# Kernel optimization log

Measured on AMD Instinct MI355X. Metric: run time of the kernel, lower is better.

Reference implementation:

```python
import jax, jax.numpy as jnp
import numpy as np
from jax.ops import segment_sum, segment_max

# Graph layout: B contiguous graphs of NPER nodes each
N, B, NPER, E, K = 32768, 32, 1024, 524288, 32
IN_DIM, HID = 64, 64
H1, H2 = 4, 2
NEG_ATTN, NEG_ACT = 0.2, 0.01  # DGL GATConv leaky slope; module's LeakyReLU slope


def _gat(x, src, dst, W, al, ar, H, D):
    # DGL GATConv, no bias, no residual, dropout=0
    f = (x @ W).reshape(N, H, D)                      # [N,H,D]
    el = jnp.einsum('nhd,hd->nh', f, al)              # src attention term
    er = jnp.einsum('nhd,hd->nh', f, ar)              # dst attention term
    e = jax.nn.leaky_relu(el[src] + er[dst], NEG_ATTN)  # [E,H]
    m = segment_max(e, dst, num_segments=N)
    m = jnp.where(jnp.isfinite(m), m, 0.0)            # guard isolated nodes
    p = jnp.exp(e - m[dst])
    z = segment_sum(p, dst, num_segments=N)
    a = p / jnp.maximum(z[dst], 1e-9)                 # edge softmax over in-edges
    return segment_sum(a[:, :, None] * f[src], dst, num_segments=N)  # [N,H,D]


def _graphnorm(x, alpha, gamma, beta, eps=1e-5):
    # GraphNorm (Cai et al.): per-graph node normalization with learnable mean scale
    xb = x.reshape(B, NPER, *x.shape[1:])
    mean = xb.mean(axis=1, keepdims=True)
    c = xb - alpha * mean
    var = (c * c).mean(axis=1, keepdims=True)
    return (gamma * c / jnp.sqrt(var + eps) + beta).reshape(x.shape)


def _sortpool(x):
    # DGL SortPooling: sort each node's features ascending, pick top-K nodes by last channel
    xs = jnp.sort(x, axis=-1).reshape(B, NPER, -1)
    _, idx = jax.lax.top_k(xs[:, :, -1], K)           # [B,K]
    sel = jnp.take_along_axis(xs, idx[:, :, None], axis=1)  # [B,K,D]
    return sel.reshape(B, -1)


def setup_inputs() -> dict:
    key = jax.random.key(0)
    ks = jax.random.split(key, 16)
    rng = np.random.default_rng(0)
    # edges constrained within each contiguous graph block
    g = rng.integers(0, B, size=E)
    src = (g * NPER + rng.integers(0, NPER, size=E)).astype(np.int32)
    dst = (g * NPER + rng.integers(0, NPER, size=E)).astype(np.int32)
    s = 0.05
    return {
        'features': jax.random.normal(ks[0], (N, IN_DIM), jnp.float32),
        'src': jnp.asarray(src), 'dst': jnp.asarray(dst),
        'W1': jax.random.normal(ks[1], (IN_DIM, H1 * HID), jnp.float32) * s,
        'al1': jax.random.normal(ks[2], (H1, HID), jnp.float32) * s,
        'ar1': jax.random.normal(ks[3], (H1, HID), jnp.float32) * s,
        'W2': jax.random.normal(ks[4], (H1 * HID, H2 * HID), jnp.float32) * s,
        'al2': jax.random.normal(ks[5], (H2, HID), jnp.float32) * s,
        'ar2': jax.random.normal(ks[6], (H2, HID), jnp.float32) * s,
        'gn1_alpha': jnp.ones((HID,), jnp.float32),
        'gn1_gamma': jnp.ones((HID,), jnp.float32),
        'gn1_beta': jnp.zeros((HID,), jnp.float32),
        'gn2_alpha': jnp.ones((HID,), jnp.float32),
        'gn2_gamma': jnp.ones((HID,), jnp.float32),
        'gn2_beta': jnp.zeros((HID,), jnp.float32),
        'fc1_w': jax.random.normal(ks[7], (2 * K * HID, K * HID), jnp.float32) * 0.02,
        'fc1_b': jnp.zeros((K * HID,), jnp.float32),
        'fc2_w': jax.random.normal(ks[8], (K * HID, 16), jnp.float32) * 0.02,
        'fc2_b': jnp.zeros((16,), jnp.float32),
    }


def reference(features, src, dst, W1, al1, ar1, W2, al2, ar2,
              gn1_alpha, gn1_gamma, gn1_beta, gn2_alpha, gn2_gamma, gn2_beta,
              fc1_w, fc1_b, fc2_w, fc2_b):
    h1 = _gat(features, src, dst, W1, al1, ar1, H1, HID)          # [N,4,HID]
    h1 = jax.nn.leaky_relu(_graphnorm(h1, gn1_alpha, gn1_gamma, gn1_beta), NEG_ACT)
    r1 = _sortpool(h1.mean(1))                                    # [B,K*HID]
    h2 = _gat(h1.reshape(N, -1), src, dst, W2, al2, ar2, H2, HID)  # [N,2,HID]
    h2 = jax.nn.leaky_relu(_graphnorm(h2, gn2_alpha, gn2_gamma, gn2_beta), NEG_ACT)
    r = jnp.concatenate([r1, _sortpool(h2.mean(1))], axis=1)      # [B,2*K*HID]
    hidden = jax.nn.relu(r @ fc1_w + fc1_b)
    return hidden @ fc2_w + fc2_b                                 # [B,16]
```

## Files before the change

kernel.cpp:

```cpp
#include <hip/hip_runtime.h>
#include <math.h>

#define NNODES 32768
#define NGRAPH 32
#define NPERG  1024
#define KSEL   32
#define FC1_KS 64

__device__ inline float wave_reduce_sum(float v) {
  #pragma unroll
  for (int off = 32; off > 0; off >>= 1) v += __shfl_xor(v, off, 64);
  return v;
}
__device__ inline float wave_reduce_max(float v) {
  #pragma unroll
  for (int off = 32; off > 0; off >>= 1) v = fmaxf(v, __shfl_xor(v, off, 64));
  return v;
}

__global__ void csr_count(const int* __restrict__ dst, int* __restrict__ counts, int E_) {
  int e = blockIdx.x * 256 + threadIdx.x;
  if (e < E_) atomicAdd(&counts[dst[e]], 1);
}

__global__ __launch_bounds__(1024) void csr_scan(const int* __restrict__ counts,
                                                 int* __restrict__ rowptr,
                                                 int* __restrict__ cursor) {
  __shared__ int partial[1024];
  const int tid = threadIdx.x;
  const int base = tid * 32;
  int c[32];
  int s = 0;
  #pragma unroll
  for (int i = 0; i < 32; ++i) { c[i] = counts[base + i]; s += c[i]; }
  partial[tid] = s;
  __syncthreads();
  for (int off = 1; off < 1024; off <<= 1) {
    int t = (tid >= off) ? partial[tid - off] : 0;
    __syncthreads();
    partial[tid] += t;
    __syncthreads();
  }
  int run = partial[tid] - s;
  #pragma unroll
  for (int i = 0; i < 32; ++i) {
    rowptr[base + i] = run;
    cursor[base + i] = run;
    run += c[i];
  }
  if (tid == 1023) rowptr[NNODES] = run;
}

__global__ void csr_fill(const int* __restrict__ src, const int* __restrict__ dst,
                         int* __restrict__ cursor, int* __restrict__ csrsrc, int E_) {
  int e = blockIdx.x * 256 + threadIdx.x;
  if (e < E_) {
    int p = atomicAdd(&cursor[dst[e]], 1);
    csrsrc[p] = src[e];
  }
}

template <int K, int C, int H>
__global__ __launch_bounds__(256) void gemm_fused(
    const float* __restrict__ X, const float* __restrict__ W,
    const float* __restrict__ al, const float* __restrict__ ar,
    float* __restrict__ F, float* __restrict__ el, float* __restrict__ er) {
  __shared__ float Xs[16][68];
  __shared__ float Ws[16][64];
  __shared__ float redl[64][16];
  __shared__ float redr[64][16];
  const int tid = threadIdx.x;
  const int tx = tid & 15, ty = tid >> 4;
  const int bx = blockIdx.x;
  const int xcd = bx & 7, pos = bx >> 3;
  const int gph = xcd + (pos >> 4) * 8;
  const int row0 = (gph * 16 + (pos & 15)) * 64;
  const int col0 = blockIdx.y * 64;

  float acc[4][4];
  #pragma unroll
  for (int i = 0; i < 4; ++i)
    #pragma unroll
    for (int j = 0; j < 4; ++j) acc[i][j] = 0.f;

  const int rld = tid >> 2;
  const int kq = (tid & 3) * 4;
  const int kw = tid >> 4;
  const int cw = (tid & 15) * 4;

  for (int kt = 0; kt < K; kt += 16) {
    float4 xv = *(const float4*)&X[(size_t)(row0 + rld) * K + kt + kq];
    Xs[kq + 0][rld] = xv.x; Xs[kq + 1][rld] = xv.y;
    Xs[kq + 2][rld] = xv.z; Xs[kq + 3][rld] = xv.w;
    *(float4*)&Ws[kw][cw] = *(const float4*)&W[(size_t)(kt + kw) * C + col0 + cw];
    __syncthreads();
    #pragma unroll
    for (int k = 0; k < 16; ++k) {
      float xr[4], wr[4];
      #pragma unroll
      for (int i = 0; i < 4; ++i) xr[i] = Xs[k][ty * 4 + i];
      #pragma unroll
      for (int j = 0; j < 4; ++j) wr[j] = Ws[k][tx * 4 + j];
      #pragma unroll
      for (int i = 0; i < 4; ++i)
        #pragma unroll
        for (int j = 0; j < 4; ++j) acc[i][j] = fmaf(xr[i], wr[j], acc[i][j]);
    }
    __syncthreads();
  }

  float av[4], rv[4];
  #pragma unroll
  for (int j = 0; j < 4; ++j) { av[j] = al[col0 + tx * 4 + j]; rv[j] = ar[col0 + tx * 4 + j]; }
  #pragma unroll
  for (int i = 0; i < 4; ++i) {
    float4 o = make_float4(acc[i][0], acc[i][1], acc[i][2], acc[i][3]);
    *(float4*)&F[(size_t)(row0 + ty * 4 + i) * C + col0 + tx * 4] = o;
    float pl = acc[i][0] * av[0] + acc[i][1] * av[1] + acc[i][2] * av[2] + acc[i][3] * av[3];
    float pr = acc[i][0] * rv[0] + acc[i][1] * rv[1] + acc[i][2] * rv[2] + acc[i][3] * rv[3];
    redl[ty * 4 + i][tx] = pl;
    redr[ty * 4 + i][tx] = pr;
  }
  __syncthreads();
  if (tid < 64) {
    float s = 0.f, t = 0.f;
    #pragma unroll
    for (int x = 0; x < 16; ++x) { s += redl[tid][x]; t += redr[tid][x]; }
    el[(row0 + tid) * H + blockIdx.y] = s;
    er[(row0 + tid) * H + blockIdx.y] = t;
  }
}

template <int H>
__device__ inline void load_ev(const float* __restrict__ el, int s, float* ev) {
  if constexpr (H == 4) {
    float4 t = *(const float4*)(el + (size_t)s * 4);
    ev[0] = t.x; ev[1] = t.y; ev[2] = t.z; ev[3] = t.w;
  } else {
    float2 t = *(const float2*)(el + (size_t)s * 2);
    ev[0] = t.x; ev[1] = t.y;
  }
}

template <int H>
__global__ __launch_bounds__(256) void gat_agg(
    const float* __restrict__ F, const float* __restrict__ el,
    const float* __restrict__ er, const int* __restrict__ rowptr,
    const int* __restrict__ csrsrc, float* __restrict__ out) {
  __shared__ float plds[4][64][H];
  __shared__ int slds[4][64];
  const int wave = threadIdx.x >> 6;
  const int lane = threadIdx.x & 63;
  const int wg = blockIdx.x;
  const int xcd = wg & 7, pos = wg >> 3;
  const int g = xcd + (pos >> 8) * 8;
  const int n = g * NPERG + (pos & 255) * 4 + wave;
  const int beg = rowptr[n], end = rowptr[n + 1];
  const int hsel = (H == 4) ? (lane >> 4) : (lane >> 5);

  float erh[H];
  #pragma unroll
  for (int h = 0; h < H; ++h) erh[h] = er[n * H + h];

  float accv[H], psum[H];
  #pragma unroll
  for (int h = 0; h < H; ++h) { accv[h] = 0.f; psum[h] = 0.f; }

  for (int cbeg = beg; cbeg < end; cbeg += 64) {
    int cnt = end - cbeg;
    if (cnt > 64) cnt = 64;
    float pv[H];
    int s = 0;
    #pragma unroll
    for (int h = 0; h < H; ++h) pv[h] = 0.f;
    if (lane < cnt) {
      s = csrsrc[cbeg + lane];
      float ev[H];
      load_ev<H>(el, s, ev);
      #pragma unroll
      for (int h = 0; h < H; ++h) {
        float e = ev[h] + erh[h];
        e = e >= 0.f ? e : 0.2f * e;
        pv[h] = __expf(e);
      }
    }
    #pragma unroll
    for (int h = 0; h < H; ++h) psum[h] += wave_reduce_sum(pv[h]);
    slds[wave][lane] = s;
    if constexpr (H == 4)
      *(float4*)&plds[wave][lane][0] = make_float4(pv[0], pv[1], pv[2], pv[3]);
    else
      *(float2*)&plds[wave][lane][0] = make_float2(pv[0], pv[1]);
    __builtin_amdgcn_s_waitcnt(0);

    int j = 0;
    for (; j + 4 <= cnt; j += 4) {
      int ss0 = slds[wave][j + 0], ss1 = slds[wave][j + 1];
      int ss2 = slds[wave][j + 2], ss3 = slds[wave][j + 3];
      float pb0 = plds[wave][j + 0][hsel], pb1 = plds[wave][j + 1][hsel];
      float pb2 = plds[wave][j + 2][hsel], pb3 = plds[wave][j + 3][hsel];
      if constexpr (H == 4) {
        float4 f0 = *(const float4*)&F[(size_t)ss0 * 256 + lane * 4];
        float4 f1 = *(const float4*)&F[(size_t)ss1 * 256 + lane * 4];
        float4 f2 = *(const float4*)&F[(size_t)ss2 * 256 + lane * 4];
        float4 f3 = *(const float4*)&F[(size_t)ss3 * 256 + lane * 4];
        accv[0] = fmaf(pb0, f0.x, accv[0]); accv[1] = fmaf(pb0, f0.y, accv[1]);
        accv[2] = fmaf(pb0, f0.z, accv[2]); accv[3] = fmaf(pb0, f0.w, accv[3]);
        accv[0] = fmaf(pb1, f1.x, accv[0]); accv[1] = fmaf(pb1, f1.y, accv[1]);
        accv[2] = fmaf(pb1, f1.z, accv[2]); accv[3] = fmaf(pb1, f1.w, accv[3]);
        accv[0] = fmaf(pb2, f2.x, accv[0]); accv[1] = fmaf(pb2, f2.y, accv[1]);
        accv[2] = fmaf(pb2, f2.z, accv[2]); accv[3] = fmaf(pb2, f2.w, accv[3]);
        accv[0] = fmaf(pb3, f3.x, accv[0]); accv[1] = fmaf(pb3, f3.y, accv[1]);
        accv[2] = fmaf(pb3, f3.z, accv[2]); accv[3] = fmaf(pb3, f3.w, accv[3]);
      } else {
        float2 f0 = *(const float2*)&F[(size_t)ss0 * 128 + lane * 2];
        float2 f1 = *(const float2*)&F[(size_t)ss1 * 128 + lane * 2];
        float2 f2 = *(const float2*)&F[(size_t)ss2 * 128 + lane * 2];
        float2 f3 = *(const float2*)&F[(size_t)ss3 * 128 + lane * 2];
        accv[0] = fmaf(pb0, f0.x, accv[0]); accv[1] = fmaf(pb0, f0.y, accv[1]);
        accv[0] = fmaf(pb1, f1.x, accv[0]); accv[1] = fmaf(pb1, f1.y, accv[1]);
        accv[0] = fmaf(pb2, f2.x, accv[0]); accv[1] = fmaf(pb2, f2.y, accv[1]);
        accv[0] = fmaf(pb3, f3.x, accv[0]); accv[1] = fmaf(pb3, f3.y, accv[1]);
      }
    }
    for (; j < cnt; ++j) {
      int ss = slds[wave][j];
      float pb = plds[wave][j][hsel];
      if constexpr (H == 4) {
        float4 fv = *(const float4*)&F[(size_t)ss * 256 + lane * 4];
        accv[0] = fmaf(pb, fv.x, accv[0]); accv[1] = fmaf(pb, fv.y, accv[1]);
        accv[2] = fmaf(pb, fv.z, accv[2]); accv[3] = fmaf(pb, fv.w, accv[3]);
      } else {
        float2 fv = *(const float2*)&F[(size_t)ss * 128 + lane * 2];
        accv[0] = fmaf(pb, fv.x, accv[0]); accv[1] = fmaf(pb, fv.y, accv[1]);
      }
    }
  }

  float z;
  if constexpr (H == 4)
    z = hsel == 0 ? psum[0] : hsel == 1 ? psum[1] : hsel == 2 ? psum[2] : psum[3];
  else
    z = hsel == 0 ? psum[0] : psum[1];
  float inv = 1.0f / fmaxf(z, 1e-9f);
  if constexpr (H == 4) {
    float4 o = make_float4(accv[0] * inv, accv[1] * inv, accv[2] * inv, accv[3] * inv);
    *(float4*)&out[(size_t)n * 256 + lane * 4] = o;
  } else {
    float2 o = make_float2(accv[0] * inv, accv[1] * inv);
    *(float2*)&out[(size_t)n * 128 + lane * 2] = o;
  }
}

template <int C>
__global__ void gn_stats_partial(const float* __restrict__ X, float* __restrict__ ps,
                                 float* __restrict__ ps2) {
  const int id = blockIdx.x;
  const int xcd = id & 7, pos = id >> 3;
  const int b = xcd + (pos >> 4) * 8;
  const int sgm = pos & 15;
  int ch = threadIdx.x;
  const float* p = X + ((size_t)b * NPERG + sgm * 64) * C + ch;
  float sx = 0.f, sx2 = 0.f;
  for (int i = 0; i < 64; ++i) { float x = p[(size_t)i * C]; sx += x; sx2 += x * x; }
  ps[(b * 16 + sgm) * C + ch] = sx;
  ps2[(b * 16 + sgm) * C + ch] = sx2;
}

template <int C>
__global__ void gn_stats_final(const float* __restrict__ ps, const float* __restrict__ ps2,
                               const float* __restrict__ alpha, const float* __restrict__ gamma,
                               const float* __restrict__ beta, float* __restrict__ scale,
                               float* __restrict__ shift) {
  int b = blockIdx.x, ch = threadIdx.x;
  float sx = 0.f, sx2 = 0.f;
  for (int s = 0; s < 16; ++s) { sx += ps[(b * 16 + s) * C + ch]; sx2 += ps2[(b * 16 + s) * C + ch]; }
  const float inv = 1.0f / (float)NPERG;
  float mu = sx * inv;
  int d = ch & 63;
  float a = alpha[d];
  float var = sx2 * inv - mu * mu * a * (2.f - a);
  float sc = gamma[d] / sqrtf(var + 1e-5f);
  scale[b * C + ch] = sc;
  shift[b * C + ch] = beta[d] - sc * a * mu;
}

__global__ void gn_apply1(const float* __restrict__ h1, const float* __restrict__ scale,
                          const float* __restrict__ shift, float* __restrict__ h1n,
                          float* __restrict__ keyb) {
  const int wg = blockIdx.x;
  const int xcd = wg & 7, pos = wg >> 3;
  const int g = xcd + (pos >> 8) * 8;
  const int n = g * NPERG + (pos & 255) * 4 + (threadIdx.x >> 6);
  const int d = threadIdx.x & 63;
  const int b = g;
  float s = 0.f;
  #pragma unroll
  for (int h = 0; h < 4; ++h) {
    int ch = h * 64 + d;
    float y = scale[b * 256 + ch] * h1[(size_t)n * 256 + ch] + shift[b * 256 + ch];
    y = y >= 0.f ? y : 0.01f * y;
    h1n[(size_t)n * 256 + ch] = y;
    s += y;
  }
  float key = wave_reduce_max(0.25f * s);
  if (d == 0) keyb[n] = key;
}

__global__ void gn_apply2(const float* __restrict__ h2, const float* __restrict__ scale,
                          const float* __restrict__ shift, float* __restrict__ keyb) {
  const int wg = blockIdx.x;
  const int xcd = wg & 7, pos = wg >> 3;
  const int g = xcd + (pos >> 8) * 8;
  const int n = g * NPERG + (pos & 255) * 4 + (threadIdx.x >> 6);
  const int d = threadIdx.x & 63;
  const int b = g;
  float s = 0.f;
  #pragma unroll
  for (int h = 0; h < 2; ++h) {
    int ch = h * 64 + d;
    float y = scale[b * 128 + ch] * h2[(size_t)n * 128 + ch] + shift[b * 128 + ch];
    y = y >= 0.f ? y : 0.01f * y;
    s += y;
  }
  float key = wave_reduce_max(0.5f * s);
  if (d == 0) keyb[n] = key;
}

__device__ inline float bitonic_sort64(float v, int lane) {
  #pragma unroll
  for (int kk = 2; kk <= 64; kk <<= 1) {
    #pragma unroll
    for (int j = kk >> 1; j > 0; j >>= 1) {
      float o = __shfl_xor(v, j, 64);
      bool lower = (lane & j) == 0;
      bool asc = (lane & kk) == 0;
      v = (lower == asc) ? fminf(v, o) : fmaxf(v, o);
    }
  }
  return v;
}

__device__ inline void bitonic_sort1024(unsigned long long& v,
                                        unsigned long long* lds, int tid) {
  for (int kk = 2; kk <= NPERG; kk <<= 1) {
    for (int j = kk >> 1; j > 0; j >>= 1) {
      unsigned long long o;
      if (j >= 64) {
        lds[tid] = v;
        __syncthreads();
        o = lds[tid ^ j];
        __syncthreads();
      } else {
        o = __shfl_xor(v, j, 64);
      }
      bool lower = (tid & j) == 0;
      bool desc = (tid & kk) == 0;
      unsigned long long mx = v > o ? v : o;
      unsigned long long mn = v > o ? o : v;
      v = (lower == desc) ? mx : mn;
    }
  }
  lds[tid] = v;
  __syncthreads();
}

__device__ inline unsigned long long pack_key(float f, int tid) {
  unsigned int u = __float_as_uint(f);
  u = (u & 0x80000000u) ? ~u : (u | 0x80000000u);
  return ((unsigned long long)u << 32) | (unsigned int)(NPERG - 1 - tid);
}

__global__ __launch_bounds__(1024) void topk_pool1(const float* __restrict__ keyb,
                                                   const float* __restrict__ h1n,
                                                   float* __restrict__ r) {
  __shared__ unsigned long long lds[NPERG];
  const int b = blockIdx.x, tid = threadIdx.x;
  unsigned long long v = pack_key(keyb[b * NPERG + tid], tid);
  bitonic_sort1024(v, lds, tid);
  const int wave = tid >> 6, lane = tid & 63;
  #pragma unroll
  for (int q = 0; q < 2; ++q) {
    int rank = wave * 2 + q;
    int node = (int)(NPERG - 1 - (unsigned int)(lds[rank] & 0xFFFFFFFFu));
    size_t base = ((size_t)(b * NPERG + node)) * 256;
    float s = 0.f;
    #pragma unroll
    for (int h = 0; h < 4; ++h) s += h1n[base + h * 64 + lane];
    float val = bitonic_sort64(0.25f * s, lane);
    r[(size_t)b * 4096 + rank * 64 + lane] = val;
  }
}

__global__ __launch_bounds__(1024) void topk_pool2(const float* __restrict__ keyb,
                                                   const float* __restrict__ h2,
                                                   const float* __restrict__ scale,
                                                   const float* __restrict__ shift,
                                                   float* __restrict__ r) {
  __shared__ unsigned long long lds[NPERG];
  const int b = blockIdx.x, tid = threadIdx.x;
  unsigned long long v = pack_key(keyb[b * NPERG + tid], tid);
  bitonic_sort1024(v, lds, tid);
  const int wave = tid >> 6, lane = tid & 63;
  #pragma unroll
  for (int q = 0; q < 2; ++q) {
    int rank = wave * 2 + q;
    int node = (int)(NPERG - 1 - (unsigned int)(lds[rank] & 0xFFFFFFFFu));
    size_t base = ((size_t)(b * NPERG + node)) * 128;
    float s = 0.f;
    #pragma unroll
    for (int h = 0; h < 2; ++h) {
      int ch = h * 64 + lane;
      float y = scale[b * 128 + ch] * h2[base + ch] + shift[b * 128 + ch];
      y = y >= 0.f ? y : 0.01f * y;
      s += y;
    }
    float val = bitonic_sort64(0.5f * s, lane);
    r[(size_t)b * 4096 + 2048 + rank * 64 + lane] = val;
  }
}

__global__ __launch_bounds__(256) void fc1_partial(const float* __restrict__ r,
                                                   const float* __restrict__ w,
                                                   float* __restrict__ part) {
  __shared__ float rs_t[64][36];
  const int ks = blockIdx.x, nb = blockIdx.y;
  const int tid = threadIdx.x;
  const int tx = tid & 63;
  const int ty = tid >> 6;

  #pragma unroll
  for (int t = 0; t < 8; ++t) {
    int elem = t * 256 + tid;
    int m = elem >> 6, k = elem & 63;
    rs_t[k][m] = r[(size_t)m * 4096 + ks * 64 + k];
  }
  __syncthreads();

  const float* wp = w + (size_t)(ks * 64) * 2048 + nb * 256 + tx * 4;
  float4 acc[8];
  #pragma unroll
  for (int i = 0; i < 8; ++i) acc[i] = make_float4(0.f, 0.f, 0.f, 0.f);

  #pragma unroll 4
  for (int k = 0; k < 64; ++k) {
    float4 wv = *(const float4*)&wp[(size_t)k * 2048];
    float4 ra = *(const float4*)&rs_t[k][ty * 8];
    float4 rb = *(const float4*)&rs_t[k][ty * 8 + 4];
    float rr[8] = {ra.x, ra.y, ra.z, ra.w, rb.x, rb.y, rb.z, rb.w};
    #pragma unroll
    for (int i = 0; i < 8; ++i) {
      acc[i].x = fmaf(rr[i], wv.x, acc[i].x);
      acc[i].y = fmaf(rr[i], wv.y, acc[i].y);
      acc[i].z = fmaf(rr[i], wv.z, acc[i].z);
      acc[i].w = fmaf(rr[i], wv.w, acc[i].w);
    }
  }

  #pragma unroll
  for (int i = 0; i < 8; ++i) {
    int m = ty * 8 + i;
    *(float4*)&part[((size_t)ks * 32 + m) * 2048 + nb * 256 + tx * 4] = acc[i];
  }
}

__global__ __launch_bounds__(256) void fc1_reduce(const float* __restrict__ part,
                                                  const float* __restrict__ bias,
                                                  float* __restrict__ hidden) {
  int idx = blockIdx.x * 256 + threadIdx.x;
  int m = idx >> 9, n4 = idx & 511;
  const float* pp = part + (size_t)m * 2048 + n4 * 4;
  float4 b4 = *(const float4*)&bias[n4 * 4];
  float4 s = b4;
  #pragma unroll 8
  for (int ks = 0; ks < FC1_KS; ++ks) {
    float4 v = *(const float4*)&pp[(size_t)ks * 32 * 2048];
    s.x += v.x; s.y += v.y; s.z += v.z; s.w += v.w;
  }
  s.x = fmaxf(s.x, 0.f); s.y = fmaxf(s.y, 0.f);
  s.z = fmaxf(s.z, 0.f); s.w = fmaxf(s.w, 0.f);
  *(float4*)&hidden[(size_t)m * 2048 + n4 * 4] = s;
}

__global__ void fc2_kernel(const float* __restrict__ hidden, const float* __restrict__ w,
                           const float* __restrict__ bias, float* __restrict__ out) {
  int wid = (blockIdx.x * blockDim.x + threadIdx.x) >> 6;
  int lane = threadIdx.x & 63;
  int m = wid >> 4, o = wid & 15;
  float s = 0.f;
  for (int k = lane; k < 2048; k += 64) s = fmaf(hidden[(size_t)m * 2048 + k], w[k * 16 + o], s);
  s = wave_reduce_sum(s);
  if (lane == 0) out[m * 16 + o] = s + bias[o];
}

extern "C" void kernel_launch(void* const* d_in, const int* in_sizes, int n_in,
                              void* d_out, int out_size, void* d_ws, size_t ws_size,
                              hipStream_t stream) {
  const float* features = (const float*)d_in[0];
  const int* src = (const int*)d_in[1];
  const int* dst = (const int*)d_in[2];
  const float* W1 = (const float*)d_in[3];
  const float* al1 = (const float*)d_in[4];
  const float* ar1 = (const float*)d_in[5];
  const float* W2 = (const float*)d_in[6];
  const float* al2 = (const float*)d_in[7];
  const float* ar2 = (const float*)d_in[8];
  const float* gn1a = (const float*)d_in[9];
  const float* gn1g = (const float*)d_in[10];
  const float* gn1b = (const float*)d_in[11];
  const float* gn2a = (const float*)d_in[12];
  const float* gn2g = (const float*)d_in[13];
  const float* gn2b = (const float*)d_in[14];
  const float* fc1w = (const float*)d_in[15];
  const float* fc1b = (const float*)d_in[16];
  const float* fc2w = (const float*)d_in[17];
  const float* fc2b = (const float*)d_in[18];
  float* out = (float*)d_out;
  const int E_ = in_sizes[1];

  float* ws = (float*)d_ws;
  size_t off = 0;
  float* A = ws + off;      off += (size_t)NNODES * 256;
  float* Bb = ws + off;     off += (size_t)NNODES * 256;
  float* el1 = ws + off;    off += (size_t)NNODES * 4;
  float* er1 = ws + off;    off += (size_t)NNODES * 4;
  float* el2 = ws + off;    off += (size_t)NNODES * 2;
  float* er2 = ws + off;    off += (size_t)NNODES * 2;
  float* sc1 = ws + off;    off += 32 * 256;
  float* sh1 = ws + off;    off += 32 * 256;
  float* sc2 = ws + off;    off += 32 * 128;
  float* sh2 = ws + off;    off += 32 * 128;
  float* ps = ws + off;     off += 32 * 16 * 256;
  float* ps2 = ws + off;    off += 32 * 16 * 256;
  float* rbuf = ws + off;   off += 32 * 4096;
  float* keyb = ws + off;   off += NNODES;
  int* ibase = (int*)(ws + off);
  int* counts = ibase;
  int* rowptr = counts + NNODES;
  int* cursor = rowptr + NNODES + 1;
  int* csrsrc = cursor + NNODES;

  float* f1 = A;
  float* h1n = A;
  float* h1 = Bb;
  float* f2 = Bb;
  float* h2 = Bb + (size_t)NNODES * 128;
  float* part = A;
  float* hidden = A + (size_t)FC1_KS * 32 * 2048;

  hipMemsetAsync(counts, 0, NNODES * sizeof(int), stream);
  csr_count<<<(E_ + 255) / 256, 256, 0, stream>>>(dst, counts, E_);
  csr_scan<<<1, 1024, 0, stream>>>(counts, rowptr, cursor);
  csr_fill<<<(E_ + 255) / 256, 256, 0, stream>>>(src, dst, cursor, csrsrc, E_);

  dim3 g1(NNODES / 64, 4);
  gemm_fused<64, 256, 4><<<g1, 256, 0, stream>>>(features, W1, al1, ar1, f1, el1, er1);
  gat_agg<4><<<NNODES / 4, 256, 0, stream>>>(f1, el1, er1, rowptr, csrsrc, h1);

  gn_stats_partial<256><<<NGRAPH * 16, 256, 0, stream>>>(h1, ps, ps2);
  gn_stats_final<256><<<NGRAPH, 256, 0, stream>>>(ps, ps2, gn1a, gn1g, gn1b, sc1, sh1);
  gn_apply1<<<NNODES / 4, 256, 0, stream>>>(h1, sc1, sh1, h1n, keyb);

  topk_pool1<<<NGRAPH, 1024, 0, stream>>>(keyb, h1n, rbuf);

  dim3 g2(NNODES / 64, 2);
  gemm_fused<256, 128, 2><<<g2, 256, 0, stream>>>(h1n, W2, al2, ar2, f2, el2, er2);
  gat_agg<2><<<NNODES / 4, 256, 0, stream>>>(f2, el2, er2, rowptr, csrsrc, h2);

  gn_stats_partial<128><<<NGRAPH * 16, 128, 0, stream>>>(h2, ps, ps2);
  gn_stats_final<128><<<NGRAPH, 128, 0, stream>>>(ps, ps2, gn2a, gn2g, gn2b, sc2, sh2);
  gn_apply2<<<NNODES / 4, 256, 0, stream>>>(h2, sc2, sh2, keyb);

  topk_pool2<<<NGRAPH, 1024, 0, stream>>>(keyb, h2, sc2, sh2, rbuf);

  dim3 gfc(FC1_KS, 8);
  fc1_partial<<<gfc, 256, 0, stream>>>(rbuf, fc1w, part);
  fc1_reduce<<<32 * 2048 / 1024, 256, 0, stream>>>(part, fc1b, hidden);
  fc2_kernel<<<128, 256, 0, stream>>>(hidden, fc2w, fc2b, out);
}
```

Measured before the change: 259.6 us.

## Fuse GraphNorm apply into layer-2 GEMM and drop normalized h1 buffer

The GraphNorm scale/shift and LeakyReLU for layer 1 are now applied on the fly in the X-load of a new layer-2 GEMM kernel and in topk_pool1, instead of writing a normalized h1n tensor. The gn_apply kernels become a shared key-only kernel that writes no feature data. This removes a 32 MB write plus a re-read of the normalized activations, in exchange for recomputing the normalization inside the GEMM tile loads. The new GEMM also uses a full 128-column tile per block with XCD-aware graph mapping, so one block covers both heads, and the buffer aliasing is reorganized.

Result: no change. 258.0 us (-0.6%).

```diff
diff --git a/kernel.cpp b/kernel.cpp
--- a/kernel.cpp
+++ b/kernel.cpp
@@ -128,6 +128,90 @@
     for (int x = 0; x < 16; ++x) { s += redl[tid][x]; t += redr[tid][x]; }
     el[(row0 + tid) * H + blockIdx.y] = s;
     er[(row0 + tid) * H + blockIdx.y] = t;
+  }
+}
+
+__global__ __launch_bounds__(256) void gemm2_fused(
+    const float* __restrict__ X, const float* __restrict__ sc,
+    const float* __restrict__ sh, const float* __restrict__ W,
+    const float* __restrict__ al, const float* __restrict__ ar,
+    float* __restrict__ F, float* __restrict__ el, float* __restrict__ er) {
+  __shared__ float Xs[16][68];
+  __shared__ float Ws[16][128];
+  __shared__ float redl[2][64][8];
+  __shared__ float redr[2][64][8];
+  const int tid = threadIdx.x;
+  const int tx = tid & 15, ty = tid >> 4;
+  const int bx = blockIdx.x;
+  const int xcd = bx & 7, pos = bx >> 3;
+  const int gph = xcd + (pos >> 4) * 8;
+  const int row0 = (gph * 16 + (pos & 15)) * 64;
+  const int b = gph;
+
+  float acc[4][8];
+  #pragma unroll
+  for (int i = 0; i < 4; ++i)
+    #pragma unroll
+    for (int j = 0; j < 8; ++j) acc[i][j] = 0.f;
+
+  const int rld = tid >> 2;
+  const int kq = (tid & 3) * 4;
+  const int kw = tid >> 4;
+  const int cw = (tid & 15) * 8;
+
+  for (int kt = 0; kt < 256; kt += 16) {
+    float4 xv = *(const float4*)&X[(size_t)(row0 + rld) * 256 + kt + kq];
+    float4 scv = *(const float4*)&sc[b * 256 + kt + kq];
+    float4 shv = *(const float4*)&sh[b * 256 + kt + kq];
+    float y0 = fmaf(scv.x, xv.x, shv.x); y0 = y0 >= 0.f ? y0 : 0.01f * y0;
+    float y1 = fmaf(scv.y, xv.y, shv.y); y1 = y1 >= 0.f ? y1 : 0.01f * y1;
+    float y2 = fmaf(scv.z, xv.z, shv.z); y2 = y2 >= 0.f ? y2 : 0.01f * y2;
+    float y3 = fmaf(scv.w, xv.w, shv.w); y3 = y3 >= 0.f ? y3 : 0.01f * y3;
+    Xs[kq + 0][rld] = y0; Xs[kq + 1][rld] = y1;
+    Xs[kq + 2][rld] = y2; Xs[kq + 3][rld] = y3;
+    *(float4*)&Ws[kw][cw] = *(const float4*)&W[(size_t)(kt + kw) * 128 + cw];
+    *(float4*)&Ws[kw][cw + 4] = *(const float4*)&W[(size_t)(kt + kw) * 128 + cw + 4];
+    __syncthreads();
+    #pragma unroll
+    for (int k = 0; k < 16; ++k) {
+      float xr[4], wr[8];
+      #pragma unroll
+      for (int i = 0; i < 4; ++i) xr[i] = Xs[k][ty * 4 + i];
+      #pragma unroll
+      for (int j = 0; j < 8; ++j) wr[j] = Ws[k][tx * 8 + j];
+      #pragma unroll
+      for (int i = 0; i < 4; ++i)
+        #pragma unroll
+        for (int j = 0; j < 8; ++j) acc[i][j] = fmaf(xr[i], wr[j], acc[i][j]);
+    }
+    __syncthreads();
+  }
+
+  const int hh = tx >> 3, xi = tx & 7;
+  float av[8], rv[8];
+  #pragma unroll
+  for (int j = 0; j < 8; ++j) { av[j] = al[tx * 8 + j]; rv[j] = ar[tx * 8 + j]; }
+  #pragma unroll
+  for (int i = 0; i < 4; ++i) {
+    int row = row0 + ty * 4 + i;
+    *(float4*)&F[(size_t)row * 128 + tx * 8] =
+        make_float4(acc[i][0], acc[i][1], acc[i][2], acc[i][3]);
+    *(float4*)&F[(size_t)row * 128 + tx * 8 + 4] =
+        make_float4(acc[i][4], acc[i][5], acc[i][6], acc[i][7]);
+    float pl = 0.f, pr = 0.f;
+    #pragma unroll
+    for (int j = 0; j < 8; ++j) { pl = fmaf(acc[i][j], av[j], pl); pr = fmaf(acc[i][j], rv[j], pr); }
+    redl[hh][ty * 4 + i][xi] = pl;
+    redr[hh][ty * 4 + i][xi] = pr;
+  }
+  __syncthreads();
+  if (tid < 128) {
+    int row = tid & 63, h = tid >> 6;
+    float s = 0.f, t = 0.f;
+    #pragma unroll
+    for (int x = 0; x < 8; ++x) { s += redl[h][row][x]; t += redr[h][row][x]; }
+    el[(row0 + row) * 2 + h] = s;
+    er[(row0 + row) * 2 + h] = t;
   }
 }
 
@@ -285,9 +369,9 @@
   shift[b * C + ch] = beta[d] - sc * a * mu;
 }
 
-__global__ void gn_apply1(const float* __restrict__ h1, const float* __restrict__ scale,
-                          const float* __restrict__ shift, float* __restrict__ h1n,
-                          float* __restrict__ keyb) {
+template <int C, int H>
+__global__ void gn_keys(const float* __restrict__ X, const float* __restrict__ scale,
+                        const float* __restrict__ shift, float* __restrict__ keyb) {
   const int wg = blockIdx.x;
   const int xcd = wg & 7, pos = wg >> 3;
   const int g = xcd + (pos >> 8) * 8;
@@ -296,34 +380,13 @@
   const int b = g;
   float s = 0.f;
   #pragma unroll
-  for (int h = 0; h < 4; ++h) {
+  for (int h = 0; h < H; ++h) {
     int ch = h * 64 + d;
-    float y = scale[b * 256 + ch] * h1[(size_t)n * 256 + ch] + shift[b * 256 + ch];
-    y = y >= 0.f ? y : 0.01f * y;
-    h1n[(size_t)n * 256 + ch] = y;
-    s += y;
-  }
-  float key = wave_reduce_max(0.25f * s);
-  if (d == 0) keyb[n] = key;
-}
-
-__global__ void gn_apply2(const float* __restrict__ h2, const float* __restrict__ scale,
-                          const float* __restrict__ shift, float* __restrict__ keyb) {
-  const int wg = blockIdx.x;
-  const int xcd = wg & 7, pos = wg >> 3;
-  const int g = xcd + (pos >> 8) * 8;
-  const int n = g * NPERG + (pos & 255) * 4 + (threadIdx.x >> 6);
-  const int d = threadIdx.x & 63;
-  const int b = g;
-  float s = 0.f;
-  #pragma unroll
-  for (int h = 0; h < 2; ++h) {
-    int ch = h * 64 + d;
-    float y = scale[b * 128 + ch] * h2[(size_t)n * 128 + ch] + shift[b * 128 + ch];
+    float y = fmaf(scale[b * C + ch], X[(size_t)n * C + ch], shift[b * C + ch]);
     y = y >= 0.f ? y : 0.01f * y;
     s += y;
   }
-  float key = wave_reduce_max(0.5f * s);
+  float key = wave_reduce_max(s * (1.0f / H));
   if (d == 0) keyb[n] = key;
 }
 
@@ -372,7 +435,9 @@
 }
 
 __global__ __launch_bounds__(1024) void topk_pool1(const float* __restrict__ keyb,
-                                                   const float* __restrict__ h1n,
+                                                   const float* __restrict__ h1,
+                                                   const float* __restrict__ scale,
+                                                   const float* __restrict__ shift,
                                                    float* __restrict__ r) {
   __shared__ unsigned long long lds[NPERG];
   const int b = blockIdx.x, tid = threadIdx.x;
@@ -386,7 +451,12 @@
     size_t base = ((size_t)(b * NPERG + node)) * 256;
     float s = 0.f;
     #pragma unroll
-    for (int h = 0; h < 4; ++h) s += h1n[base + h * 64 + lane];
+    for (int h = 0; h < 4; ++h) {
+      int ch = h * 64 + lane;
+      float y = fmaf(scale[b * 256 + ch], h1[base + ch], shift[b * 256 + ch]);
+      y = y >= 0.f ? y : 0.01f * y;
+      s += y;
+    }
     float val = bitonic_sort64(0.25f * s, lane);
     r[(size_t)b * 4096 + rank * 64 + lane] = val;
   }
@@ -411,7 +481,7 @@
     #pragma unroll
     for (int h = 0; h < 2; ++h) {
       int ch = h * 64 + lane;
-      float y = scale[b * 128 + ch] * h2[base + ch] + shift[b * 128 + ch];
+      float y = fmaf(scale[b * 128 + ch], h2[base + ch], shift[b * 128 + ch]);
       y = y >= 0.f ? y : 0.01f * y;
       s += y;
     }
@@ -541,12 +611,11 @@
   int* csrsrc = cursor + NNODES;
 
   float* f1 = A;
-  float* h1n = A;
   float* h1 = Bb;
-  float* f2 = Bb;
-  float* h2 = Bb + (size_t)NNODES * 128;
+  float* f2 = A;
+  float* h2 = A + (size_t)NNODES * 128;
   float* part = A;
-  float* hidden = A + (size_t)FC1_KS * 32 * 2048;
+  float* hidden = Bb;
 
   hipMemsetAsync(counts, 0, NNODES * sizeof(int), stream);
   csr_count<<<(E_ + 255) / 256, 256, 0, stream>>>(dst, counts, E_);
@@ -559,17 +628,16 @@
 
   gn_stats_partial<256><<<NGRAPH * 16, 256, 0, stream>>>(h1, ps, ps2);
   gn_stats_final<256><<<NGRAPH, 256, 0, stream>>>(ps, ps2, gn1a, gn1g, gn1b, sc1, sh1);
-  gn_apply1<<<NNODES / 4, 256, 0, stream>>>(h1, sc1, sh1, h1n, keyb);
-
-  topk_pool1<<<NGRAPH, 1024, 0, stream>>>(keyb, h1n, rbuf);
-
-  dim3 g2(NNODES / 64, 2);
-  gemm_fused<256, 128, 2><<<g2, 256, 0, stream>>>(h1n, W2, al2, ar2, f2, el2, er2);
+  gn_keys<256, 4><<<NNODES / 4, 256, 0, stream>>>(h1, sc1, sh1, keyb);
+
+  topk_pool1<<<NGRAPH, 1024, 0, stream>>>(keyb, h1, sc1, sh1, rbuf);
+
+  gemm2_fused<<<NNODES / 64, 256, 0, stream>>>(h1, sc1, sh1, W2, al2, ar2, f2, el2, er2);
   gat_agg<2><<<NNODES / 4, 256, 0, stream>>>(f2, el2, er2, rowptr, csrsrc, h2);
 
   gn_stats_partial<128><<<NGRAPH * 16, 128, 0, stream>>>(h2, ps, ps2);
   gn_stats_final<128><<<NGRAPH, 128, 0, stream>>>(ps, ps2, gn2a, gn2g, gn2b, sc2, sh2);
-  gn_apply2<<<NNODES / 4, 256, 0, stream>>>(h2, sc2, sh2, keyb);
+  gn_keys<128, 2><<<NNODES / 4, 256, 0, stream>>>(h2, sc2, sh2, keyb);
 
   topk_pool2<<<NGRAPH, 1024, 0, stream>>>(keyb, h2, sc2, sh2, rbuf);
 
```
